# Kernel optimization log

Measured on AMD Instinct MI355X. Metric: run time of the kernel, lower is better.

Reference implementation:

```python
import jax, jax.numpy as jnp
import numpy as np

N_NODES = 50000
N_EDGES = 800000
IN_CH = 128
HID = 128
OUT_CH = 64
BN_EPS = 1e-5


def setup_inputs() -> dict:
    key = jax.random.key(0)
    ks = jax.random.split(key, 12)
    glorot = lambda k, fi, fo: jax.random.normal(k, (fi, fo), jnp.float32) * np.sqrt(2.0 / (fi + fo))
    return {
        "x": jax.random.normal(ks[0], (N_NODES, IN_CH), jnp.float32),
        "edge_index": jax.random.randint(ks[1], (2, N_EDGES), 0, N_NODES, jnp.int64),
        "W1": glorot(ks[2], IN_CH, HID), "b1": jnp.zeros((HID,), jnp.float32),
        "gamma1": jnp.ones((HID,), jnp.float32), "beta1": jnp.zeros((HID,), jnp.float32),
        "W2": glorot(ks[3], HID, HID), "b2": jnp.zeros((HID,), jnp.float32),
        "gamma2": jnp.ones((HID,), jnp.float32), "beta2": jnp.zeros((HID,), jnp.float32),
        "Wmu": glorot(ks[4], HID, OUT_CH), "bmu": jnp.zeros((OUT_CH,), jnp.float32),
        "Wls": glorot(ks[5], HID, OUT_CH), "bls": jnp.zeros((OUT_CH,), jnp.float32),
    }


def _gcn(h, W, b, src, dst, norm, n):
    # GCNConv: linear transform, then normalized scatter-add aggregation
    h = h @ W                                    # [N, out]
    msg = h[src] * norm[:, None]                 # [E+N, out] gathered messages
    out = jax.ops.segment_sum(msg, dst, num_segments=n)
    return out + b


def _batch_norm(h, gamma, beta):
    mu = jnp.mean(h, axis=0)
    var = jnp.mean(jnp.square(h - mu), axis=0)   # biased var (BatchNorm1d train mode)
    return (h - mu) * jax.lax.rsqrt(var + BN_EPS) * gamma + beta


def reference(x, edge_index, W1, b1, gamma1, beta1, W2, b2, gamma2, beta2, Wmu, bmu, Wls, bls):
    n = x.shape[0]
    loops = jnp.arange(n, dtype=edge_index.dtype)
    src = jnp.concatenate([edge_index[0], loops])  # add self-loops
    dst = jnp.concatenate([edge_index[1], loops])
    # symmetric normalization deg^-1/2 A_hat deg^-1/2 (same for every layer)
    deg = jax.ops.segment_sum(jnp.ones_like(src, jnp.float32), dst, num_segments=n)
    dinv = jax.lax.rsqrt(deg)                     # deg >= 1 because of self-loops
    norm = dinv[src] * dinv[dst]

    h = jax.nn.relu(_batch_norm(_gcn(x, W1, b1, src, dst, norm, n), gamma1, beta1))
    h = jax.nn.relu(_batch_norm(_gcn(h, W2, b2, src, dst, norm, n), gamma2, beta2))
    mu = _gcn(h, Wmu, bmu, src, dst, norm, n)
    logstd = _gcn(h, Wls, bls, src, dst, norm, n)
    return (mu, logstd)
```

## Files before the change

kernel.cpp:

```cpp
#include <hip/hip_runtime.h>

#define NN 50000
#define NE 800000
#define C 128
#define OUTC 64
#define BN_EPS 1e-5f
#define INVN (1.0f / 50000.0f)
#define NBLK 49

typedef __attribute__((ext_vector_type(8))) short bf16x8;
typedef __attribute__((ext_vector_type(4))) float f32x4;
typedef __attribute__((ext_vector_type(8))) unsigned short u16x8;

__device__ __forceinline__ unsigned short f2bf(float f) {
    unsigned u = __float_as_uint(f);
    u += 0x7fffu + ((u >> 16) & 1u);
    return (unsigned short)(u >> 16);
}
__device__ __forceinline__ float bf2f(unsigned short s) {
    return __uint_as_float((unsigned)s << 16);
}


__global__ __launch_bounds__(256) void hist_kernel(const int* __restrict__ dstp, int* __restrict__ cnt) {
    int e = blockIdx.x * 256 + threadIdx.x;
    if (e < NE) atomicAdd(&cnt[dstp[e]], 1);
}

__global__ __launch_bounds__(256) void scan1_kernel(const int* __restrict__ cnt, int* __restrict__ rowptr,
                                                    float* __restrict__ dinv, int* __restrict__ bsum) {
    __shared__ int lds[256];
    int tid = threadIdx.x;
    int base = blockIdx.x * 1024 + tid * 4;
    int v[4];
    int s = 0;
    #pragma unroll
    for (int j = 0; j < 4; ++j) { int i = base + j; v[j] = (i < NN) ? cnt[i] : 0; s += v[j]; }
    lds[tid] = s;
    __syncthreads();
    for (int off = 1; off < 256; off <<= 1) {
        int x = (tid >= off) ? lds[tid - off] : 0;
        __syncthreads();
        lds[tid] += x;
        __syncthreads();
    }
    int excl = lds[tid] - s;
    #pragma unroll
    for (int j = 0; j < 4; ++j) {
        int i = base + j;
        if (i < NN) {
            rowptr[i] = excl;
            dinv[i] = rsqrtf((float)(v[j] + 1));
        }
        excl += v[j];
    }
    if (tid == 255) bsum[blockIdx.x] = lds[255];
}

__global__ __launch_bounds__(256) void scan3_kernel(const int* __restrict__ bsum, int* __restrict__ rowptr,
                                                    int* __restrict__ wpos) {
    __shared__ int boff;
    int tid = threadIdx.x;
    if (tid < 64) {
        int orig = (tid < NBLK) ? bsum[tid] : 0;
        int v = orig;
        #pragma unroll
        for (int off = 1; off < 64; off <<= 1) {
            int x = __shfl_up(v, off);
            if (tid >= off) v += x;
        }
        if (tid == (int)blockIdx.x) boff = v - orig;
    }
    __syncthreads();
    int off = boff;
    int base = blockIdx.x * 1024 + tid * 4;
    #pragma unroll
    for (int j = 0; j < 4; ++j) {
        int i = base + j;
        if (i < NN) { int r = rowptr[i] + off; rowptr[i] = r; wpos[i] = r; }
    }
    if (blockIdx.x == 0 && tid == 0) rowptr[NN] = NE;
}

__global__ __launch_bounds__(256) void fill_kernel(const int* __restrict__ srcp, const int* __restrict__ dstp,
                                                   int* __restrict__ wpos, int* __restrict__ col) {
    int e = blockIdx.x * 256 + threadIdx.x;
    if (e < NE) {
        int d = dstp[e];
        int p = atomicAdd(&wpos[d], 1);
        col[p] = srcp[e];
    }
}


__global__ __launch_bounds__(256) void prep_kernel(const float* __restrict__ W1, const float* __restrict__ W2,
                                                   const float* __restrict__ Wmu, const float* __restrict__ Wls,
                                                   unsigned short* __restrict__ Wpk) {
    int idx = blockIdx.x * 256 + threadIdx.x;
    if (idx >= 3 * 2048) return;
    int which = idx >> 11;
    int r = idx & 2047;
    int l = r & 63;
    int nt = (r >> 6) & 7;
    int kt = r >> 9;
    int m = l & 15, kg = l >> 4;
    int c = nt * 16 + m;
    bf16x8 o;
    #pragma unroll
    for (int j = 0; j < 8; ++j) {
        int k = kt * 32 + kg * 8 + j;
        float w;
        if (which == 0)      w = W1[k * 128 + c];
        else if (which == 1) w = W2[k * 128 + c];
        else                 w = (c < 64) ? Wmu[k * 64 + c] : Wls[k * 64 + (c - 64)];
        o[j] = (short)f2bf(w);
    }
    *(bf16x8*)&Wpk[(size_t)which * 16384 + (size_t)r * 8] = o;
}


template<bool TRANS>
__global__ __launch_bounds__(256) void gemm_kernel(
    const float* __restrict__ A, const unsigned short* __restrict__ Wpk,
    const float* __restrict__ sums, const float* __restrict__ gamma, const float* __restrict__ beta,
    const float* __restrict__ dinv, unsigned short* __restrict__ out)
{
    int tid = threadIdx.x;
    int wv = tid >> 6, l = tid & 63;
    int m = l & 15, kg = l >> 4;
    int rhalf = wv & 1, chalf = wv >> 1;
    int row = blockIdx.x * 32 + rhalf * 16 + m;
    int rowc = min(row, NN - 1);
    const float* Ar = A + (size_t)rowc * C;

    f32x4 acc[4] = {};

    #pragma unroll
    for (int kt = 0; kt < 4; ++kt) {
        int k0 = kt * 32 + kg * 8;
        float4 x0 = *(const float4*)&Ar[k0];
        float4 x1 = *(const float4*)&Ar[k0 + 4];
        float av[8] = {x0.x, x0.y, x0.z, x0.w, x1.x, x1.y, x1.z, x1.w};
        if (TRANS) {
            #pragma unroll
            for (int j = 0; j < 8; ++j) {
                int k = k0 + j;
                float mean = sums[k] * INVN;
                float var = fmaf(-mean, mean, sums[128 + k] * INVN);
                float sc = gamma[k] * rsqrtf(var + BN_EPS);
                float sh = fmaf(-mean, sc, beta[k]);
                av[j] = fmaxf(fmaf(av[j], sc, sh), 0.f);
            }
        }
        bf16x8 af;
        #pragma unroll
        for (int j = 0; j < 8; ++j) af[j] = (short)f2bf(av[j]);
        #pragma unroll
        for (int n = 0; n < 4; ++n) {
            int nt = chalf * 4 + n;
            bf16x8 bfr = *(const bf16x8*)&Wpk[(size_t)((kt * 8 + nt) * 64 + l) * 8];
            acc[n] = __builtin_amdgcn_mfma_f32_16x16x32_bf16(af, bfr, acc[n], 0, 0, 0);
        }
    }

    int ro = blockIdx.x * 32 + rhalf * 16 + kg * 4;
    #pragma unroll
    for (int r = 0; r < 4; ++r) {
        int orow = ro + r;
        if (orow < NN) {
            float di = dinv[orow];
            #pragma unroll
            for (int n = 0; n < 4; ++n)
                out[(size_t)orow * C + (chalf * 4 + n) * 16 + m] = f2bf(di * acc[n][r]);
        }
    }
}


template<bool SPLIT>
__global__ __launch_bounds__(256) void agg_kernel(
    const unsigned short* __restrict__ t, const int* __restrict__ rowptr, const int* __restrict__ col,
    const float* __restrict__ dinv, const float* __restrict__ bmu, const float* __restrict__ bls,
    float* __restrict__ outb, float* __restrict__ out2)
{
    int wave = threadIdx.x >> 6, lane = threadIdx.x & 63;
    int row = blockIdx.x * 4 + wave;
    int q = lane & 15, eg = lane >> 4;
    const unsigned short* tq = t + q * 8;
    int e0 = rowptr[row], e1 = rowptr[row + 1];
    float a[8] = {};

    for (int e = e0; e < e1; e += 16) {
        int lim = e1 - 1;
        u16x8 v[4];
        float msk[4];
        #pragma unroll
        for (int b = 0; b < 4; ++b) {
            int i = e + b * 4 + eg;
            msk[b] = (i < e1) ? 1.f : 0.f;
            if (e + b * 4 < e1) {
                int s = col[min(i, lim)];
                v[b] = *(const u16x8*)&tq[(size_t)s * C];
            } else {
                v[b] = (u16x8)0;
                msk[b] = 0.f;
            }
        }
        #pragma unroll
        for (int b = 0; b < 4; ++b) {
            #pragma unroll
            for (int j = 0; j < 8; ++j)
                a[j] = fmaf(msk[b], bf2f(v[b][j]), a[j]);
        }
    }

    {
        u16x8 vs = *(const u16x8*)&tq[(size_t)row * C];
        float ms = (eg == 0) ? 1.f : 0.f;
        #pragma unroll
        for (int j = 0; j < 8; ++j)
            a[j] = fmaf(ms, bf2f(vs[j]), a[j]);
    }

    #pragma unroll
    for (int j = 0; j < 8; ++j) {
        a[j] += __shfl_xor(a[j], 16);
        a[j] += __shfl_xor(a[j], 32);
    }

    if (eg == 0) {
        float di = dinv[row];
        int c = q * 8;
        if (!SPLIT) {
            *(float4*)&outb[(size_t)row * C + c]     = make_float4(di*a[0], di*a[1], di*a[2], di*a[3]);
            *(float4*)&outb[(size_t)row * C + c + 4] = make_float4(di*a[4], di*a[5], di*a[6], di*a[7]);
        } else {
            if (c < 64) {
                float4 b0 = *(const float4*)&bmu[c];
                float4 b1 = *(const float4*)&bmu[c + 4];
                *(float4*)&outb[(size_t)row * OUTC + c]
                    = make_float4(fmaf(di,a[0],b0.x), fmaf(di,a[1],b0.y), fmaf(di,a[2],b0.z), fmaf(di,a[3],b0.w));
                *(float4*)&outb[(size_t)row * OUTC + c + 4]
                    = make_float4(fmaf(di,a[4],b1.x), fmaf(di,a[5],b1.y), fmaf(di,a[6],b1.z), fmaf(di,a[7],b1.w));
            } else {
                int cc = c - 64;
                float4 b0 = *(const float4*)&bls[cc];
                float4 b1 = *(const float4*)&bls[cc + 4];
                *(float4*)&out2[(size_t)row * OUTC + cc]
                    = make_float4(fmaf(di,a[0],b0.x), fmaf(di,a[1],b0.y), fmaf(di,a[2],b0.z), fmaf(di,a[3],b0.w));
                *(float4*)&out2[(size_t)row * OUTC + cc + 4]
                    = make_float4(fmaf(di,a[4],b1.x), fmaf(di,a[5],b1.y), fmaf(di,a[6],b1.z), fmaf(di,a[7],b1.w));
            }
        }
    }
}


__global__ __launch_bounds__(256) void bnstats_kernel(const float* __restrict__ h, float* __restrict__ sums) {
    int c = threadIdx.x & 127;
    int hh = threadIdx.x >> 7;
    float s = 0.f, sq = 0.f;
    for (int r = blockIdx.x * 2 + hh; r < NN; r += gridDim.x * 2) {
        float v = h[(size_t)r * C + c];
        s += v; sq = fmaf(v, v, sq);
    }
    __shared__ float ls[256], lq[256];
    ls[threadIdx.x] = s; lq[threadIdx.x] = sq;
    __syncthreads();
    if (hh == 0) {
        atomicAdd(&sums[c], s + ls[c + 128]);
        atomicAdd(&sums[128 + c], sq + lq[c + 128]);
    }
}


extern "C" void kernel_launch(void* const* d_in, const int* in_sizes, int n_in,
                              void* d_out, int out_size, void* d_ws, size_t ws_size,
                              hipStream_t stream) {
    (void)in_sizes; (void)n_in; (void)out_size; (void)ws_size;
    const float* x      = (const float*)d_in[0];
    const int*   ei     = (const int*)d_in[1];
    const float* W1     = (const float*)d_in[2];
    const float* gamma1 = (const float*)d_in[4];
    const float* beta1  = (const float*)d_in[5];
    const float* W2     = (const float*)d_in[6];
    const float* gamma2 = (const float*)d_in[8];
    const float* beta2  = (const float*)d_in[9];
    const float* Wmu    = (const float*)d_in[10];
    const float* bmu    = (const float*)d_in[11];
    const float* Wls    = (const float*)d_in[12];
    const float* bls    = (const float*)d_in[13];

    float* outmu = (float*)d_out;
    float* outls = outmu + (size_t)NN * OUTC;

    char* w = (char*)d_ws;
    size_t off = 0;
    auto alloc = [&](size_t bytes) { char* p = w + off; off = (off + bytes + 255) & ~(size_t)255; return p; };
    unsigned short* t = (unsigned short*)alloc(sizeof(unsigned short) * NN * C);
    float* aggb   = (float*)alloc(sizeof(float) * NN * C);
    int*   cnt    = (int*)  alloc(sizeof(int) * NN);
    float* sums   = (float*)alloc(sizeof(float) * 512);
    int*   rowptr = (int*)  alloc(sizeof(int) * (NN + 1));
    int*   wpos   = (int*)  alloc(sizeof(int) * NN);
    int*   col    = (int*)  alloc(sizeof(int) * NE);
    float* dinv   = (float*)alloc(sizeof(float) * NN);
    int*   bsum   = (int*)  alloc(sizeof(int) * 64);
    unsigned short* Wpk = (unsigned short*)alloc(sizeof(unsigned short) * 3 * 16384);
    float* sumsA = sums; float* sumsB = sums + 256;

    const int* srcp = ei;
    const int* dstp = ei + NE;

    size_t zspan = (size_t)((char*)(sums + 512) - (char*)cnt);
    hipMemsetAsync(cnt, 0, zspan, stream);

    hist_kernel<<<(NE + 255) / 256, 256, 0, stream>>>(dstp, cnt);
    scan1_kernel<<<NBLK, 256, 0, stream>>>(cnt, rowptr, dinv, bsum);
    scan3_kernel<<<NBLK, 256, 0, stream>>>(bsum, rowptr, wpos);
    fill_kernel<<<(NE + 255) / 256, 256, 0, stream>>>(srcp, dstp, wpos, col);
    prep_kernel<<<24, 256, 0, stream>>>(W1, W2, Wmu, Wls, Wpk);

    const int GB = (NN + 31) / 32;
    const int AB = NN / 4;

    gemm_kernel<false><<<GB, 256, 0, stream>>>(x, Wpk, nullptr, nullptr, nullptr, dinv, t);
    agg_kernel<false><<<AB, 256, 0, stream>>>(t, rowptr, col, dinv, nullptr, nullptr, aggb, nullptr);
    bnstats_kernel<<<400, 256, 0, stream>>>(aggb, sumsA);

    gemm_kernel<true><<<GB, 256, 0, stream>>>(aggb, Wpk + 16384, sumsA, gamma1, beta1, dinv, t);
    agg_kernel<false><<<AB, 256, 0, stream>>>(t, rowptr, col, dinv, nullptr, nullptr, aggb, nullptr);
    bnstats_kernel<<<400, 256, 0, stream>>>(aggb, sumsB);

    gemm_kernel<true><<<GB, 256, 0, stream>>>(aggb, Wpk + 32768, sumsB, gamma2, beta2, dinv, t);
    agg_kernel<true><<<AB, 256, 0, stream>>>(t, rowptr, col, dinv, bmu, bls, outmu, outls);
}
```

Measured before the change: 408.1 us.

## Partition edges by destination shard for CSR fill and store intermediates in bf16

Replaces the global histogram and atomic fill with a two-pass partition of edges into 8 destination shards, so each fill block's atomics and col writes stay within one range of nodes for better locality. Separately, the aggregated hidden activations between layers are stored as bf16 instead of fp32. This halves the traffic for the agg writes, the bnstats reads and the next GEMM's reads. The trade-offs are extra partition kernels, a packed 64-bit edge buffer, and lost precision in the BN statistics inputs.

```diff
diff --git a/kernel.cpp b/kernel.cpp
--- a/kernel.cpp
+++ b/kernel.cpp
@@ -7,6 +7,11 @@
 #define BN_EPS 1e-5f
 #define INVN (1.0f / 50000.0f)
 #define NBLK 49
+#define NSH 8
+#define SHW (NN / NSH)
+#define NCHUNK 256
+#define CHUNK (NE / NCHUNK)
+#define FB 32
 
 typedef __attribute__((ext_vector_type(8))) short bf16x8;
 typedef __attribute__((ext_vector_type(4))) float f32x4;
@@ -22,9 +27,56 @@
 }
 
 
-__global__ __launch_bounds__(256) void hist_kernel(const int* __restrict__ dstp, int* __restrict__ cnt) {
-    int e = blockIdx.x * 256 + threadIdx.x;
-    if (e < NE) atomicAdd(&cnt[dstp[e]], 1);
+__global__ __launch_bounds__(256) void pcount_kernel(const int* __restrict__ dstp, int* __restrict__ pc) {
+    __shared__ int lc[8];
+    int tid = threadIdx.x, mb = blockIdx.x;
+    if (tid < 8) lc[tid] = 0;
+    __syncthreads();
+    int end = (mb + 1) * CHUNK;
+    for (int e = mb * CHUNK + tid; e < end; e += 256)
+        atomicAdd(&lc[dstp[e] / SHW], 1);
+    __syncthreads();
+    if (tid < 8) pc[mb * 8 + tid] = lc[tid];
+}
+
+__global__ __launch_bounds__(256) void pscan_kernel(const int* __restrict__ pc, int* __restrict__ po) {
+    __shared__ int lds[256];
+    int t = threadIdx.x;
+    int v[8], s = 0;
+    #pragma unroll
+    for (int j = 0; j < 8; ++j) {
+        int i = t * 8 + j;
+        v[j] = pc[(i & (NCHUNK - 1)) * 8 + (i >> 8)];
+        s += v[j];
+    }
+    lds[t] = s;
+    __syncthreads();
+    for (int off = 1; off < 256; off <<= 1) {
+        int x = (t >= off) ? lds[t - off] : 0;
+        __syncthreads();
+        lds[t] += x;
+        __syncthreads();
+    }
+    int excl = lds[t] - s;
+    #pragma unroll
+    for (int j = 0; j < 8; ++j) { po[t * 8 + j] = excl; excl += v[j]; }
+}
+
+__global__ __launch_bounds__(256) void ppart_kernel(const int* __restrict__ srcp, const int* __restrict__ dstp,
+                                                    const int* __restrict__ po,
+                                                    unsigned long long* __restrict__ part, int* __restrict__ cnt) {
+    __shared__ int base[8], ctr[8];
+    int tid = threadIdx.x, mb = blockIdx.x;
+    if (tid < 8) { base[tid] = po[tid * NCHUNK + mb]; ctr[tid] = 0; }
+    __syncthreads();
+    int end = (mb + 1) * CHUNK;
+    for (int e = mb * CHUNK + tid; e < end; e += 256) {
+        int d = dstp[e], s = srcp[e];
+        atomicAdd(&cnt[d], 1);
+        int g = d / SHW;
+        int slot = atomicAdd(&ctr[g], 1);
+        part[(size_t)(base[g] + slot)] = ((unsigned long long)(unsigned)d << 32) | (unsigned)s;
+    }
 }
 
 __global__ __launch_bounds__(256) void scan1_kernel(const int* __restrict__ cnt, int* __restrict__ rowptr,
@@ -82,13 +134,17 @@
     if (blockIdx.x == 0 && tid == 0) rowptr[NN] = NE;
 }
 
-__global__ __launch_bounds__(256) void fill_kernel(const int* __restrict__ srcp, const int* __restrict__ dstp,
-                                                   int* __restrict__ wpos, int* __restrict__ col) {
-    int e = blockIdx.x * 256 + threadIdx.x;
-    if (e < NE) {
-        int d = dstp[e];
+__global__ __launch_bounds__(256) void fill2_kernel(const unsigned long long* __restrict__ part,
+                                                    const int* __restrict__ po,
+                                                    int* __restrict__ wpos, int* __restrict__ col) {
+    int g = blockIdx.x & 7, ib = blockIdx.x >> 3;
+    int lo = po[g * NCHUNK];
+    int hi = (g == 7) ? NE : po[(g + 1) * NCHUNK];
+    for (int idx = lo + ib * 256 + threadIdx.x; idx < hi; idx += FB * 256) {
+        unsigned long long pk = part[idx];
+        int d = (int)(pk >> 32), s = (int)(pk & 0xffffffffu);
         int p = atomicAdd(&wpos[d], 1);
-        col[p] = srcp[e];
+        col[p] = s;
     }
 }
 
@@ -121,7 +177,7 @@
 
 template<bool TRANS>
 __global__ __launch_bounds__(256) void gemm_kernel(
-    const float* __restrict__ A, const unsigned short* __restrict__ Wpk,
+    const void* __restrict__ Av, const unsigned short* __restrict__ Wpk,
     const float* __restrict__ sums, const float* __restrict__ gamma, const float* __restrict__ beta,
     const float* __restrict__ dinv, unsigned short* __restrict__ out)
 {
@@ -131,17 +187,16 @@
     int rhalf = wv & 1, chalf = wv >> 1;
     int row = blockIdx.x * 32 + rhalf * 16 + m;
     int rowc = min(row, NN - 1);
-    const float* Ar = A + (size_t)rowc * C;
 
     f32x4 acc[4] = {};
 
     #pragma unroll
     for (int kt = 0; kt < 4; ++kt) {
         int k0 = kt * 32 + kg * 8;
-        float4 x0 = *(const float4*)&Ar[k0];
-        float4 x1 = *(const float4*)&Ar[k0 + 4];
-        float av[8] = {x0.x, x0.y, x0.z, x0.w, x1.x, x1.y, x1.z, x1.w};
+        bf16x8 af;
         if (TRANS) {
+            const unsigned short* Ar = (const unsigned short*)Av + (size_t)rowc * C;
+            u16x8 raw = *(const u16x8*)&Ar[k0];
             #pragma unroll
             for (int j = 0; j < 8; ++j) {
                 int k = k0 + j;
@@ -149,12 +204,17 @@
                 float var = fmaf(-mean, mean, sums[128 + k] * INVN);
                 float sc = gamma[k] * rsqrtf(var + BN_EPS);
                 float sh = fmaf(-mean, sc, beta[k]);
-                av[j] = fmaxf(fmaf(av[j], sc, sh), 0.f);
+                af[j] = (short)f2bf(fmaxf(fmaf(bf2f(raw[j]), sc, sh), 0.f));
             }
-        }
-        bf16x8 af;
-        #pragma unroll
-        for (int j = 0; j < 8; ++j) af[j] = (short)f2bf(av[j]);
+        } else {
+            const float* Ar = (const float*)Av + (size_t)rowc * C;
+            float4 x0 = *(const float4*)&Ar[k0];
+            float4 x1 = *(const float4*)&Ar[k0 + 4];
+            af[0] = (short)f2bf(x0.x); af[1] = (short)f2bf(x0.y);
+            af[2] = (short)f2bf(x0.z); af[3] = (short)f2bf(x0.w);
+            af[4] = (short)f2bf(x1.x); af[5] = (short)f2bf(x1.y);
+            af[6] = (short)f2bf(x1.z); af[7] = (short)f2bf(x1.w);
+        }
         #pragma unroll
         for (int n = 0; n < 4; ++n) {
             int nt = chalf * 4 + n;
@@ -181,7 +241,7 @@
 __global__ __launch_bounds__(256) void agg_kernel(
     const unsigned short* __restrict__ t, const int* __restrict__ rowptr, const int* __restrict__ col,
     const float* __restrict__ dinv, const float* __restrict__ bmu, const float* __restrict__ bls,
-    float* __restrict__ outb, float* __restrict__ out2)
+    unsigned short* __restrict__ outb16, float* __restrict__ outmu, float* __restrict__ outls)
 {
     int wave = threadIdx.x >> 6, lane = threadIdx.x & 63;
     int row = blockIdx.x * 4 + wave;
@@ -232,23 +292,25 @@
         float di = dinv[row];
         int c = q * 8;
         if (!SPLIT) {
-            *(float4*)&outb[(size_t)row * C + c]     = make_float4(di*a[0], di*a[1], di*a[2], di*a[3]);
-            *(float4*)&outb[(size_t)row * C + c + 4] = make_float4(di*a[4], di*a[5], di*a[6], di*a[7]);
+            u16x8 o;
+            #pragma unroll
+            for (int j = 0; j < 8; ++j) o[j] = f2bf(di * a[j]);
+            *(u16x8*)&outb16[(size_t)row * C + c] = o;
         } else {
             if (c < 64) {
                 float4 b0 = *(const float4*)&bmu[c];
                 float4 b1 = *(const float4*)&bmu[c + 4];
-                *(float4*)&outb[(size_t)row * OUTC + c]
+                *(float4*)&outmu[(size_t)row * OUTC + c]
                     = make_float4(fmaf(di,a[0],b0.x), fmaf(di,a[1],b0.y), fmaf(di,a[2],b0.z), fmaf(di,a[3],b0.w));
-                *(float4*)&outb[(size_t)row * OUTC + c + 4]
+                *(float4*)&outmu[(size_t)row * OUTC + c + 4]
                     = make_float4(fmaf(di,a[4],b1.x), fmaf(di,a[5],b1.y), fmaf(di,a[6],b1.z), fmaf(di,a[7],b1.w));
             } else {
                 int cc = c - 64;
                 float4 b0 = *(const float4*)&bls[cc];
                 float4 b1 = *(const float4*)&bls[cc + 4];
-                *(float4*)&out2[(size_t)row * OUTC + cc]
+                *(float4*)&outls[(size_t)row * OUTC + cc]
                     = make_float4(fmaf(di,a[0],b0.x), fmaf(di,a[1],b0.y), fmaf(di,a[2],b0.z), fmaf(di,a[3],b0.w));
-                *(float4*)&out2[(size_t)row * OUTC + cc + 4]
+                *(float4*)&outls[(size_t)row * OUTC + cc + 4]
                     = make_float4(fmaf(di,a[4],b1.x), fmaf(di,a[5],b1.y), fmaf(di,a[6],b1.z), fmaf(di,a[7],b1.w));
             }
         }
@@ -256,12 +318,12 @@
 }
 
 
-__global__ __launch_bounds__(256) void bnstats_kernel(const float* __restrict__ h, float* __restrict__ sums) {
+__global__ __launch_bounds__(256) void bnstats_kernel(const unsigned short* __restrict__ h, float* __restrict__ sums) {
     int c = threadIdx.x & 127;
     int hh = threadIdx.x >> 7;
     float s = 0.f, sq = 0.f;
     for (int r = blockIdx.x * 2 + hh; r < NN; r += gridDim.x * 2) {
-        float v = h[(size_t)r * C + c];
+        float v = bf2f(h[(size_t)r * C + c]);
         s += v; sq = fmaf(v, v, sq);
     }
     __shared__ float ls[256], lq[256];
@@ -297,8 +359,8 @@
     char* w = (char*)d_ws;
     size_t off = 0;
     auto alloc = [&](size_t bytes) { char* p = w + off; off = (off + bytes + 255) & ~(size_t)255; return p; };
-    unsigned short* t = (unsigned short*)alloc(sizeof(unsigned short) * NN * C);
-    float* aggb   = (float*)alloc(sizeof(float) * NN * C);
+    unsigned short* t    = (unsigned short*)alloc(sizeof(unsigned short) * NN * C);
+    unsigned short* aggb = (unsigned short*)alloc(sizeof(unsigned short) * NN * C);
     int*   cnt    = (int*)  alloc(sizeof(int) * NN);
     float* sums   = (float*)alloc(sizeof(float) * 512);
     int*   rowptr = (int*)  alloc(sizeof(int) * (NN + 1));
@@ -306,6 +368,9 @@
     int*   col    = (int*)  alloc(sizeof(int) * NE);
     float* dinv   = (float*)alloc(sizeof(float) * NN);
     int*   bsum   = (int*)  alloc(sizeof(int) * 64);
+    int*   pc     = (int*)  alloc(sizeof(int) * NCHUNK * 8);
+    int*   po     = (int*)  alloc(sizeof(int) * NCHUNK * 8);
+    unsigned long long* part = (unsigned long long*)alloc(sizeof(unsigned long long) * NE);
     unsigned short* Wpk = (unsigned short*)alloc(sizeof(unsigned short) * 3 * 16384);
     float* sumsA = sums; float* sumsB = sums + 256;
 
@@ -315,23 +380,25 @@
     size_t zspan = (size_t)((char*)(sums + 512) - (char*)cnt);
     hipMemsetAsync(cnt, 0, zspan, stream);
 
-    hist_kernel<<<(NE + 255) / 256, 256, 0, stream>>>(dstp, cnt);
+    pcount_kernel<<<NCHUNK, 256, 0, stream>>>(dstp, pc);
+    pscan_kernel<<<1, 256, 0, stream>>>(pc, po);
+    ppart_kernel<<<NCHUNK, 256, 0, stream>>>(srcp, dstp, po, part, cnt);
     scan1_kernel<<<NBLK, 256, 0, stream>>>(cnt, rowptr, dinv, bsum);
     scan3_kernel<<<NBLK, 256, 0, stream>>>(bsum, rowptr, wpos);
-    fill_kernel<<<(NE + 255) / 256, 256, 0, stream>>>(srcp, dstp, wpos, col);
+    fill2_kernel<<<NSH * FB, 256, 0, stream>>>(part, po, wpos, col);
     prep_kernel<<<24, 256, 0, stream>>>(W1, W2, Wmu, Wls, Wpk);
 
     const int GB = (NN + 31) / 32;
     const int AB = NN / 4;
 
     gemm_kernel<false><<<GB, 256, 0, stream>>>(x, Wpk, nullptr, nullptr, nullptr, dinv, t);
-    agg_kernel<false><<<AB, 256, 0, stream>>>(t, rowptr, col, dinv, nullptr, nullptr, aggb, nullptr);
+    agg_kernel<false><<<AB, 256, 0, stream>>>(t, rowptr, col, dinv, nullptr, nullptr, aggb, nullptr, nullptr);
     bnstats_kernel<<<400, 256, 0, stream>>>(aggb, sumsA);
 
     gemm_kernel<true><<<GB, 256, 0, stream>>>(aggb, Wpk + 16384, sumsA, gamma1, beta1, dinv, t);
-    agg_kernel<false><<<AB, 256, 0, stream>>>(t, rowptr, col, dinv, nullptr, nullptr, aggb, nullptr);
+    agg_kernel<false><<<AB, 256, 0, stream>>>(t, rowptr, col, dinv, nullptr, nullptr, aggb, nullptr, nullptr);
     bnstats_kernel<<<400, 256, 0, stream>>>(aggb, sumsB);
 
     gemm_kernel<true><<<GB, 256, 0, stream>>>(aggb, Wpk + 32768, sumsB, gamma2, beta2, dinv, t);
-    agg_kernel<true><<<AB, 256, 0, stream>>>(t, rowptr, col, dinv, bmu, bls, outmu, outls);
-}
+    agg_kernel<true><<<AB, 256, 0, stream>>>(t, rowptr, col, dinv, bmu, bls, nullptr, outmu, outls);
+}
```

New measurement: 397.2 us. 2.7% less time.
